# Optimization experiments

Measured on AMD Instinct MI355X. Metric: run time of the kernel, lower is better.

Reference implementation:

```python
import jax, jax.numpy as jnp
import numpy as np
from jax import lax

B, CIN, H, W = 2, 64, 56, 56
CMID, COUT = 128, 128


def _pos_enc(h, w, c, dtype):
    # 2D sinusoidal encoding: first half of channels encode row, second half column.
    def enc1d(L, dim):
        pos = jnp.arange(L, dtype=jnp.float32)[:, None]
        div = jnp.exp(-jnp.log(10000.0) * jnp.arange(0, dim, 2, dtype=jnp.float32) / dim)
        ang = pos * div
        e = jnp.zeros((L, dim), jnp.float32)
        e = e.at[:, 0::2].set(jnp.sin(ang)).at[:, 1::2].set(jnp.cos(ang))
        return e
    ch = c // 2
    eh = enc1d(h, ch)            # (H, ch)
    ew = enc1d(w, c - ch)        # (W, c-ch)
    pe = jnp.concatenate([
        jnp.broadcast_to(eh[:, None, :], (h, w, ch)),
        jnp.broadcast_to(ew[None, :, :], (h, w, c - ch)),
    ], axis=-1)
    return pe.astype(dtype)


def _nbr_idx(L, k, d):
    # NATTEN-style dilated neighborhood indices with border clamping, per dilation
    # residue group. Returns (L, k) int32 indices into [0, L).
    i = jnp.arange(L)
    p, r = i // d, i % d
    Lg = (L - r - 1) // d + 1                      # group length per residue
    start = jnp.clip(p - k // 2, 0, jnp.maximum(Lg - k, 0))
    j = jnp.arange(k)
    idx = r[:, None] + (start[:, None] + j[None, :]) * d
    return jnp.minimum(idx, L - 1)


def setup_inputs() -> dict:
    key = jax.random.key(0)
    ks = jax.random.split(key, 9)
    s3 = 1.0 / np.sqrt(CIN * 9)
    s1 = 1.0 / np.sqrt(CMID)
    return {
        "x": jax.random.normal(ks[0], (B, CIN, H, W), jnp.float32),
        "conv_w": jax.random.normal(ks[1], (CMID, CIN, 3, 3), jnp.float32) * s3,
        "conv_b": jax.random.normal(ks[2], (CMID,), jnp.float32) * 0.01,
        "q_w": jax.random.normal(ks[3], (CMID, CMID), jnp.float32) * s1,
        "q_b": jax.random.normal(ks[4], (CMID,), jnp.float32) * 0.01,
        "k_w": jax.random.normal(ks[5], (CMID, CMID), jnp.float32) * s1,
        "k_b": jax.random.normal(ks[6], (CMID,), jnp.float32) * 0.01,
        "v_w": jax.random.normal(ks[7], (COUT, CMID), jnp.float32) * s1,
        "v_b": jax.random.normal(ks[8], (COUT,), jnp.float32) * 0.01,
        "kernel_size": 7,
        "dilation": 2,
    }


def reference(x, conv_w, conv_b, q_w, q_b, k_w, k_b, v_w, v_b, kernel_size, dilation):
    # shared 3x3 conv projection (SAME padding), NCHW
    sf = lax.conv_general_dilated(x, conv_w, (1, 1), 'SAME',
                                  dimension_numbers=('NCHW', 'OIHW', 'NCHW'))
    sf = sf + conv_b[None, :, None, None]
    sf = jnp.transpose(sf, (0, 2, 3, 1))                      # (B,H,W,Cmid)
    q = jnp.einsum('bhwc,oc->bhwo', sf, q_w) + q_b            # 1x1 convs
    k = jnp.einsum('bhwc,oc->bhwo', sf, k_w) + k_b
    v = jnp.einsum('bhwc,oc->bhwo', sf, v_w) + v_b            # (B,H,W,Cout)
    pe = _pos_enc(q.shape[1], q.shape[2], q.shape[3], q.dtype)
    peb = jnp.broadcast_to(pe[None], q.shape)
    q = jnp.concatenate([q, peb], axis=-1)                    # (B,H,W,2Cmid)
    k = jnp.concatenate([k, peb], axis=-1)

    kk = int(kernel_size)
    dd = int(dilation)
    ih = _nbr_idx(q.shape[1], kk, dd)                         # (H,kk)
    iw = _nbr_idx(q.shape[2], kk, dd)                         # (W,kk)
    # gather dilated neighborhoods: (B,H,W,kk,kk,D)
    knb = k[:, ih[:, None, :, None], iw[None, :, None, :], :]
    vnb = v[:, ih[:, None, :, None], iw[None, :, None, :], :]
    scale = 1.0 / jnp.sqrt(jnp.asarray(q.shape[-1], q.dtype))
    logits = jnp.einsum('bhwd,bhwuvd->bhwuv', q, knb) * scale
    Bq, Hq, Wq = logits.shape[:3]
    attn = jax.nn.softmax(logits.reshape(Bq, Hq, Wq, kk * kk), axis=-1)
    attn = attn.reshape(Bq, Hq, Wq, kk, kk)
    out = jnp.einsum('bhwuv,bhwuvd->bhwd', attn, vnb)         # (B,H,W,Cout)
    return out
```

## Files before the change

kernel.cpp:

```cpp
#include <hip/hip_runtime.h>
#include <hip/hip_bf16.h>
#include <math.h>

#define BB   2
#define HH   56
#define WW   56
#define CIN  64
#define CMID 128

typedef short bf8_t __attribute__((ext_vector_type(8)));
typedef float f4_t  __attribute__((ext_vector_type(4)));
typedef _Float16 h2_t __attribute__((ext_vector_type(2)));
typedef _Float16 h8_t __attribute__((ext_vector_type(8)));

#define QH_OFF  0
#define KH_OFF  401408
#define V_OFF   802816
#define SF_OFF  1605632
#define AS_OFF  2408448
#define WFH_OFF 2408840
#define WFL_OFF 2445704
#define W2H_OFF 2482568
#define W2L_OFF 2507144

__device__ __forceinline__ unsigned short f2bf(float f) {
    unsigned int u = __builtin_bit_cast(unsigned int, f);
    u += 0x7fffu + ((u >> 16) & 1u);
    return (unsigned short)(u >> 16);
}
__device__ __forceinline__ float bf2f(unsigned short h) {
    unsigned int u = ((unsigned int)h) << 16;
    return __builtin_bit_cast(float, u);
}

__global__ __launch_bounds__(256) void prep_w(
    const float* __restrict__ cw, const float* __restrict__ qw,
    const float* __restrict__ kw, const float* __restrict__ vw,
    unsigned short* __restrict__ wfh, unsigned short* __restrict__ wfl,
    unsigned short* __restrict__ w2h, unsigned short* __restrict__ w2l,
    float* __restrict__ As)
{
    int idx = blockIdx.x * 256 + threadIdx.x;
    if (idx < 9 * 2 * 8 * 64 * 8) {
        int j    = idx & 7;
        int lane = (idx >> 3) & 63;
        int o16  = (idx >> 9) & 7;
        int kk32 = (idx >> 12) & 1;
        int seg  = idx >> 13;
        int o = o16 * 16 + (lane & 15);
        int c = kk32 * 32 + (lane >> 4) * 8 + j;
        float wv = cw[(o * 64 + c) * 9 + seg];
        unsigned short hi = f2bf(wv);
        wfh[idx] = hi; wfl[idx] = f2bf(wv - bf2f(hi));
    }
    if (idx < 4 * 24 * 64 * 8) {
        int j    = idx & 7;
        int lane = (idx >> 3) & 63;
        int rest = idx >> 9;
        int n16  = rest % 24;
        int kk32 = rest / 24;
        int n = n16 * 16 + (lane & 15);
        int c = kk32 * 32 + (lane >> 4) * 8 + j;
        int which = n >> 7, o = n & 127;
        const float* src = which == 0 ? qw : (which == 1 ? kw : vw);
        float wv = src[o * 128 + c];
        unsigned short hi = f2bf(wv);
        w2h[idx] = hi; w2l[idx] = f2bf(wv - bf2f(hi));
    }
    if (blockIdx.x == 288) {
        for (int t = threadIdx.x; t < 56 * 7; t += 256) {
            int i = t / 7, j = t % 7;
            int p = i >> 1;
            int start = p - 3;
            if (start < 0) start = 0;
            if (start > 21) start = 21;
            int nidx = (i & 1) + (start + j) * 2;
            float delta = (float)(i - nidx);
            float acc = 0.f;
            for (int u = 0; u < 32; ++u) {
                float d = expf(-9.210340371976184f * (float)u * 0.03125f);
                acc += cosf(delta * d);
            }
            As[t] = acc * 0.0625f;
        }
    }
}

__global__ __launch_bounds__(512) void conv_mfma(
    const float* __restrict__ x,
    const unsigned short* __restrict__ wfh, const unsigned short* __restrict__ wfl,
    const float* __restrict__ cb,
    float* __restrict__ sf)
{
    __shared__ char xsb[2][3 * 66 * 64 * 2];
    const int h   = blockIdx.x;
    const int b   = blockIdx.y;
    const int tid = threadIdx.x;

    for (int idx = tid; idx < 3 * 64 * 66; idx += 512) {
        int dh  = idx / (64 * 66);
        int rem = idx % (64 * 66);
        int c   = rem / 66;
        int row = rem % 66;
        int y   = h + dh - 1;
        int wg  = row - 1;
        float val = 0.f;
        if ((unsigned)y < HH && (unsigned)wg < WW)
            val = x[((b * CIN + c) * HH + y) * WW + wg];
        unsigned short hi = f2bf(val);
        unsigned short lo = f2bf(val - bf2f(hi));
        int byteoff = (((dh * 66 + row) * 64 + c) * 2) ^ ((row & 7) << 4);
        *(unsigned short*)(xsb[0] + byteoff) = hi;
        *(unsigned short*)(xsb[1] + byteoff) = lo;
    }
    __syncthreads();

    const int lane   = tid & 63;
    const int wid    = tid >> 6;
    const int wm     = wid >> 2;
    const int wn     = wid & 3;
    const int lane15 = lane & 15;
    const int lanehi = lane >> 4;

    f4_t acc[2][2] = {};

    for (int seg = 0; seg < 9; ++seg) {
        const int dh = seg / 3, dw = seg % 3;
#pragma unroll
        for (int kk32 = 0; kk32 < 2; ++kk32) {
            bf8_t ah[2], al[2], bh[2], bl[2];
#pragma unroll
            for (int mf = 0; mf < 2; ++mf) {
                int row = wm * 32 + mf * 16 + lane15 + dw;
                int byteoff = (((dh * 66 + row) * 64 + kk32 * 32 + lanehi * 8) * 2)
                              ^ ((row & 7) << 4);
                ah[mf] = *(const bf8_t*)(xsb[0] + byteoff);
                al[mf] = *(const bf8_t*)(xsb[1] + byteoff);
            }
#pragma unroll
            for (int nf = 0; nf < 2; ++nf) {
                int fidx = (((seg * 2 + kk32) * 8 + (wn * 2 + nf)) * 64 + lane) * 8;
                bh[nf] = *(const bf8_t*)(wfh + fidx);
                bl[nf] = *(const bf8_t*)(wfl + fidx);
            }
#pragma unroll
            for (int mf = 0; mf < 2; ++mf)
#pragma unroll
                for (int nf = 0; nf < 2; ++nf) {
                    acc[mf][nf] = __builtin_amdgcn_mfma_f32_16x16x32_bf16(
                        ah[mf], bh[nf], acc[mf][nf], 0, 0, 0);
                    acc[mf][nf] = __builtin_amdgcn_mfma_f32_16x16x32_bf16(
                        al[mf], bh[nf], acc[mf][nf], 0, 0, 0);
                    acc[mf][nf] = __builtin_amdgcn_mfma_f32_16x16x32_bf16(
                        ah[mf], bl[nf], acc[mf][nf], 0, 0, 0);
                }
        }
    }

    const int r4 = lanehi * 4;
#pragma unroll
    for (int mf = 0; mf < 2; ++mf) {
        int wr = wm * 32 + mf * 16 + r4;
#pragma unroll
        for (int nf = 0; nf < 2; ++nf) {
            int o = wn * 32 + nf * 16 + lane15;
            float bias = cb[o];
#pragma unroll
            for (int r = 0; r < 4; ++r) {
                int wpos = wr + r;
                if (wpos < 56)
                    sf[((b * HH + h) * WW + wpos) * CMID + o] = acc[mf][nf][r] + bias;
            }
        }
    }
}

__global__ __launch_bounds__(512) void qkv_mfma(
    const float* __restrict__ sf,
    const unsigned short* __restrict__ w2h, const unsigned short* __restrict__ w2l,
    const float* __restrict__ qb, const float* __restrict__ kb,
    const float* __restrict__ vb,
    _Float16* __restrict__ qh16, _Float16* __restrict__ kh16,
    float* __restrict__ vo)
{
    __shared__ char asb[2][32 * 128 * 2];
    const int p0  = blockIdx.x * 32;
    const int tid = threadIdx.x;

    {
        int row = tid >> 4;
        int c0  = (tid & 15) * 8;
        float4 fa = *(const float4*)(sf + (p0 + row) * 128 + c0);
        float4 fb = *(const float4*)(sf + (p0 + row) * 128 + c0 + 4);
        bf8_t hi, lo;
        float fv[8] = {fa.x, fa.y, fa.z, fa.w, fb.x, fb.y, fb.z, fb.w};
#pragma unroll
        for (int j = 0; j < 8; ++j) {
            unsigned short hj = f2bf(fv[j]);
            hi[j] = (short)hj;
            lo[j] = (short)f2bf(fv[j] - bf2f(hj));
        }
        int byteoff = ((row * 128 + c0) * 2) ^ ((row & 7) << 4);
        *(bf8_t*)(asb[0] + byteoff) = hi;
        *(bf8_t*)(asb[1] + byteoff) = lo;
    }
    __syncthreads();

    const int lane   = tid & 63;
    const int wid    = tid >> 6;
    const int wm     = wid >> 2;
    const int wn     = wid & 3;
    const int lane15 = lane & 15;
    const int lanehi = lane >> 4;

    f4_t acc[6] = {};

#pragma unroll
    for (int kk32 = 0; kk32 < 4; ++kk32) {
        bf8_t ah, al;
        {
            int row = wm * 16 + lane15;
            int byteoff = ((row * 128 + kk32 * 32 + lanehi * 8) * 2) ^ ((row & 7) << 4);
            ah = *(const bf8_t*)(asb[0] + byteoff);
            al = *(const bf8_t*)(asb[1] + byteoff);
        }
#pragma unroll
        for (int nf = 0; nf < 6; ++nf) {
            int fidx = ((kk32 * 24 + wn * 6 + nf) * 64 + lane) * 8;
            bf8_t bhv = *(const bf8_t*)(w2h + fidx);
            bf8_t blv = *(const bf8_t*)(w2l + fidx);
            acc[nf] = __builtin_amdgcn_mfma_f32_16x16x32_bf16(ah, bhv, acc[nf], 0, 0, 0);
            acc[nf] = __builtin_amdgcn_mfma_f32_16x16x32_bf16(al, bhv, acc[nf], 0, 0, 0);
            acc[nf] = __builtin_amdgcn_mfma_f32_16x16x32_bf16(ah, blv, acc[nf], 0, 0, 0);
        }
    }

    const int r4 = lanehi * 4;
#pragma unroll
    for (int nf = 0; nf < 6; ++nf) {
        int n = wn * 96 + nf * 16 + lane15;
        int which = n >> 7;
        int o = n & 127;
        const float* bp = which == 0 ? qb : (which == 1 ? kb : vb);
        float bias = bp[o];
        int pos = p0 + wm * 16 + r4;
#pragma unroll
        for (int r = 0; r < 4; ++r) {
            float val = acc[nf][r] + bias;
            int di = (pos + r) * CMID + o;
            if (which == 0)      qh16[di] = (_Float16)(val * 0.0625f);
            else if (which == 1) kh16[di] = (_Float16)val;
            else                 vo[di]   = val;
        }
    }
}

__global__ __launch_bounds__(256) void attn_tiled(
    const _Float16* __restrict__ qh, const _Float16* __restrict__ kh,
    const float* __restrict__ v, const float* __restrict__ As,
    float* __restrict__ out)
{
    __shared__ char Kb[112 * 256];
    __shared__ char Vb[100 * 256];
    __shared__ char Qb[16 * 256];
    __shared__ float lg[16 * 113];
    __shared__ float awv[4][64];

    const int tid = threadIdx.x;
    int bid = blockIdx.x;
    const int b   = bid / 196; bid %= 196;
    const int par = bid / 49;
    const int t49 = bid % 49;
    const int rh = par >> 1, rw = par & 1;
    const int p0 = (t49 / 7) * 4, q0 = (t49 % 7) * 4;

    int smh = p0 - 3; if (smh < 0) smh = 0; if (smh > 21) smh = 21;
    int smw = q0 - 3; if (smw < 0) smw = 0; if (smw > 21) smw = 21;

    const int rlo = tid >> 4;
    const int t16 = tid & 15;

    {
        int qi = rlo;
        int pp = p0 + (qi >> 2), qq = q0 + (qi & 3);
        int hq = rh + 2 * pp, wq = rw + 2 * qq;
        const char* src = (const char*)(qh + ((b * HH + hq) * WW + wq) * CMID);
        uint4 d = *(const uint4*)(src + t16 * 16);
        *(uint4*)(Qb + qi * 256 + ((t16 * 16) ^ ((qi & 7) << 4))) = d;
    }
    for (int r0 = 0; r0 < 112; r0 += 16) {
        int n = r0 + rlo;
        int i = n / 10, jj = n % 10;
        int ihs = smh + i; if (ihs > 27) ihs = 27;
        int iws = smw + jj; if (iws > 27) iws = 27;
        int ih = rh + 2 * ihs, iw = rw + 2 * iws;
        const char* src = (const char*)(kh + ((b * HH + ih) * WW + iw) * CMID);
        uint4 d = *(const uint4*)(src + t16 * 16);
        *(uint4*)(Kb + n * 256 + ((t16 * 16) ^ ((n & 7) << 4))) = d;
    }
    for (int r0 = 0; r0 < 112; r0 += 16) {
        int n = r0 + rlo;
        if (n < 100) {
            int i = n / 10, jj = n % 10;
            int ihs = smh + i; if (ihs > 27) ihs = 27;
            int iws = smw + jj; if (iws > 27) iws = 27;
            int ih = rh + 2 * ihs, iw = rw + 2 * iws;
            const float* src = v + ((b * HH + ih) * WW + iw) * CMID + t16 * 8;
            float4 f0 = *(const float4*)(src);
            float4 f1 = *(const float4*)(src + 4);
            h8_t d;
            d[0] = (_Float16)f0.x; d[1] = (_Float16)f0.y;
            d[2] = (_Float16)f0.z; d[3] = (_Float16)f0.w;
            d[4] = (_Float16)f1.x; d[5] = (_Float16)f1.y;
            d[6] = (_Float16)f1.z; d[7] = (_Float16)f1.w;
            *(h8_t*)(Vb + n * 256 + t16 * 16) = d;
        }
    }
    __syncthreads();

    const int lane   = tid & 63;
    const int wvid   = tid >> 6;
    const int lane15 = lane & 15;
    const int lanehi = lane >> 4;

    {
        int nfs = wvid * 2;
        int nfe = nfs + 2; if (nfe > 7) nfe = 7;
        for (int nf = nfs; nf < nfe; ++nf) {
            f4_t acc = {};
            int n = nf * 16 + lane15;
#pragma unroll
            for (int kk = 0; kk < 4; ++kk) {
                int koff = kk * 64 + lanehi * 16;
                h8_t a  = *(const h8_t*)(Qb + lane15 * 256 + (koff ^ ((lane15 & 7) << 4)));
                h8_t bb = *(const h8_t*)(Kb + n * 256      + (koff ^ ((n & 7) << 4)));
                acc = __builtin_amdgcn_mfma_f32_16x16x32_f16(a, bb, acc, 0, 0, 0);
            }
#pragma unroll
            for (int r = 0; r < 4; ++r)
                lg[(lanehi * 4 + r) * 113 + n] = acc[r];
        }
    }
    __syncthreads();

    const int u   = lane / 7;
    const int vv2 = lane % 7;

    for (int t = 0; t < 4; ++t) {
        int qi = wvid * 4 + t;
        int pp = p0 + (qi >> 2), qq = q0 + (qi & 3);
        int hq = rh + 2 * pp, wq = rw + 2 * qq;
        int sp = pp - 3; if (sp < 0) sp = 0; if (sp > 21) sp = 21;
        int sq = qq - 3; if (sq < 0) sq = 0; if (sq > 21) sq = 21;
        int ru = sp - smh, rc = sq - smw;

        float logit = -INFINITY;
        if (lane < 49) {
            int n = (ru + u) * 10 + (rc + vv2);
            logit = lg[qi * 113 + n] + As[hq * 7 + u] + As[wq * 7 + vv2];
        }
        float m = logit;
#pragma unroll
        for (int s = 32; s > 0; s >>= 1)
            m = fmaxf(m, __shfl_xor(m, s, 64));
        float e = (lane < 49) ? expf(logit - m) : 0.f;
        float ssum = e;
#pragma unroll
        for (int s = 32; s > 0; s >>= 1)
            ssum += __shfl_xor(ssum, s, 64);
        awv[wvid][lane] = e / ssum;

        float o0 = 0.f, o1 = 0.f;
#pragma unroll
        for (int u2 = 0; u2 < 7; ++u2) {
            int rowb = (ru + u2) * 10 + rc;
#pragma unroll
            for (int v2 = 0; v2 < 7; ++v2) {
                float a2 = awv[wvid][u2 * 7 + v2];
                unsigned pv = *(const unsigned*)(Vb + (rowb + v2) * 256 + lane * 4);
                h2_t ph = __builtin_bit_cast(h2_t, pv);
                o0 += a2 * (float)ph[0];
                o1 += a2 * (float)ph[1];
            }
        }
        int g = (b * HH + hq) * WW + wq;
        *(float2*)(out + g * CMID + lane * 2) = make_float2(o0, o1);
    }
}

extern "C" void kernel_launch(void* const* d_in, const int* in_sizes, int n_in,
                              void* d_out, int out_size, void* d_ws, size_t ws_size,
                              hipStream_t stream)
{
    const float* x  = (const float*)d_in[0];
    const float* cw = (const float*)d_in[1];
    const float* cb = (const float*)d_in[2];
    const float* qw = (const float*)d_in[3];
    const float* qb = (const float*)d_in[4];
    const float* kw = (const float*)d_in[5];
    const float* kb = (const float*)d_in[6];
    const float* vw = (const float*)d_in[7];
    const float* vb = (const float*)d_in[8];

    float* ws = (float*)d_ws;
    _Float16* qhx = (_Float16*)(ws + QH_OFF);
    _Float16* khx = (_Float16*)(ws + KH_OFF);
    float* vx = ws + V_OFF;
    float* sf = ws + SF_OFF;
    float* As = ws + AS_OFF;
    unsigned short* wfh = (unsigned short*)(ws + WFH_OFF);
    unsigned short* wfl = (unsigned short*)(ws + WFL_OFF);
    unsigned short* w2h = (unsigned short*)(ws + W2H_OFF);
    unsigned short* w2l = (unsigned short*)(ws + W2L_OFF);
    float* out = (float*)d_out;

    hipLaunchKernelGGL(prep_w, dim3(289), dim3(256), 0, stream,
                       cw, qw, kw, vw, wfh, wfl, w2h, w2l, As);
    hipLaunchKernelGGL(conv_mfma, dim3(56, 2), dim3(512), 0, stream,
                       x, wfh, wfl, cb, sf);
    hipLaunchKernelGGL(qkv_mfma, dim3(196), dim3(512), 0, stream,
                       sf, w2h, w2l, qb, kb, vb, qhx, khx, vx);
    hipLaunchKernelGGL(attn_tiled, dim3(392), dim3(256), 0, stream,
                       qhx, khx, vx, As, out);
}
```

Measured before the change: 132.6 us.

## Fuse conv and QKV projection into one kernel, store V as fp16

Merges the 3x3 conv and the 1x1 QKV projection into a single kernel. Each block computes a 28-wide half-row of conv output, keeps it in shared memory as split bf16 hi/lo, then runs the QKV MFMAs directly. This removes the fp32 sf round-trip through global memory and one kernel launch. V is now written as fp16, so the attention kernel copies it straight into LDS without converting, which halves V traffic. The grid doubles to 224 blocks but each block does half the conv M-tile, with some halo recompute.

```diff
diff --git a/kernel.cpp b/kernel.cpp
--- a/kernel.cpp
+++ b/kernel.cpp
@@ -15,13 +15,12 @@
 
 #define QH_OFF  0
 #define KH_OFF  401408
-#define V_OFF   802816
-#define SF_OFF  1605632
-#define AS_OFF  2408448
-#define WFH_OFF 2408840
-#define WFL_OFF 2445704
-#define W2H_OFF 2482568
-#define W2L_OFF 2507144
+#define VH_OFF  802816
+#define AS_OFF  1204224
+#define WFH_OFF 1204736
+#define WFL_OFF 1241600
+#define W2H_OFF 1278464
+#define W2L_OFF 1303040
 
 __device__ __forceinline__ unsigned short f2bf(float f) {
     unsigned int u = __builtin_bit_cast(unsigned int, f);
@@ -86,30 +85,37 @@
     }
 }
 
-__global__ __launch_bounds__(512) void conv_mfma(
+__global__ __launch_bounds__(512) void conv_qkv_mfma(
     const float* __restrict__ x,
     const unsigned short* __restrict__ wfh, const unsigned short* __restrict__ wfl,
     const float* __restrict__ cb,
-    float* __restrict__ sf)
+    const unsigned short* __restrict__ w2h, const unsigned short* __restrict__ w2l,
+    const float* __restrict__ qb, const float* __restrict__ kb,
+    const float* __restrict__ vb,
+    _Float16* __restrict__ qh16, _Float16* __restrict__ kh16,
+    _Float16* __restrict__ vh16)
 {
-    __shared__ char xsb[2][3 * 66 * 64 * 2];
-    const int h   = blockIdx.x;
-    const int b   = blockIdx.y;
+    __shared__ char xsb[2][3 * 34 * 64 * 2];
+    __shared__ char sfb[2][32 * 128 * 2];
+    const int wt = blockIdx.x;
+    const int h  = blockIdx.y;
+    const int b  = blockIdx.z;
+    const int w0 = wt * 28;
     const int tid = threadIdx.x;
 
-    for (int idx = tid; idx < 3 * 64 * 66; idx += 512) {
-        int dh  = idx / (64 * 66);
-        int rem = idx % (64 * 66);
-        int c   = rem / 66;
-        int row = rem % 66;
+    for (int idx = tid; idx < 3 * 64 * 34; idx += 512) {
+        int dh  = idx / (64 * 34);
+        int rem = idx % (64 * 34);
+        int c   = rem / 34;
+        int row = rem % 34;
         int y   = h + dh - 1;
-        int wg  = row - 1;
+        int wg  = w0 - 1 + row;
         float val = 0.f;
         if ((unsigned)y < HH && (unsigned)wg < WW)
             val = x[((b * CIN + c) * HH + y) * WW + wg];
         unsigned short hi = f2bf(val);
         unsigned short lo = f2bf(val - bf2f(hi));
-        int byteoff = (((dh * 66 + row) * 64 + c) * 2) ^ ((row & 7) << 4);
+        int byteoff = (((dh * 34 + row) * 64 + c) * 2) ^ ((row & 7) << 4);
         *(unsigned short*)(xsb[0] + byteoff) = hi;
         *(unsigned short*)(xsb[1] + byteoff) = lo;
     }
@@ -122,120 +128,63 @@
     const int lane15 = lane & 15;
     const int lanehi = lane >> 4;
 
-    f4_t acc[2][2] = {};
-
+    f4_t acc[2] = {};
     for (int seg = 0; seg < 9; ++seg) {
         const int dh = seg / 3, dw = seg % 3;
 #pragma unroll
         for (int kk32 = 0; kk32 < 2; ++kk32) {
-            bf8_t ah[2], al[2], bh[2], bl[2];
-#pragma unroll
-            for (int mf = 0; mf < 2; ++mf) {
-                int row = wm * 32 + mf * 16 + lane15 + dw;
-                int byteoff = (((dh * 66 + row) * 64 + kk32 * 32 + lanehi * 8) * 2)
-                              ^ ((row & 7) << 4);
-                ah[mf] = *(const bf8_t*)(xsb[0] + byteoff);
-                al[mf] = *(const bf8_t*)(xsb[1] + byteoff);
-            }
+            int row = wm * 16 + lane15 + dw;
+            int byteoff = (((dh * 34 + row) * 64 + kk32 * 32 + lanehi * 8) * 2)
+                          ^ ((row & 7) << 4);
+            bf8_t ah = *(const bf8_t*)(xsb[0] + byteoff);
+            bf8_t al = *(const bf8_t*)(xsb[1] + byteoff);
 #pragma unroll
             for (int nf = 0; nf < 2; ++nf) {
                 int fidx = (((seg * 2 + kk32) * 8 + (wn * 2 + nf)) * 64 + lane) * 8;
-                bh[nf] = *(const bf8_t*)(wfh + fidx);
-                bl[nf] = *(const bf8_t*)(wfl + fidx);
-            }
-#pragma unroll
-            for (int mf = 0; mf < 2; ++mf)
-#pragma unroll
-                for (int nf = 0; nf < 2; ++nf) {
-                    acc[mf][nf] = __builtin_amdgcn_mfma_f32_16x16x32_bf16(
-                        ah[mf], bh[nf], acc[mf][nf], 0, 0, 0);
-                    acc[mf][nf] = __builtin_amdgcn_mfma_f32_16x16x32_bf16(
-                        al[mf], bh[nf], acc[mf][nf], 0, 0, 0);
-                    acc[mf][nf] = __builtin_amdgcn_mfma_f32_16x16x32_bf16(
-                        ah[mf], bl[nf], acc[mf][nf], 0, 0, 0);
-                }
-        }
-    }
-
-    const int r4 = lanehi * 4;
-#pragma unroll
-    for (int mf = 0; mf < 2; ++mf) {
-        int wr = wm * 32 + mf * 16 + r4;
-#pragma unroll
-        for (int nf = 0; nf < 2; ++nf) {
-            int o = wn * 32 + nf * 16 + lane15;
-            float bias = cb[o];
-#pragma unroll
-            for (int r = 0; r < 4; ++r) {
-                int wpos = wr + r;
-                if (wpos < 56)
-                    sf[((b * HH + h) * WW + wpos) * CMID + o] = acc[mf][nf][r] + bias;
-            }
-        }
-    }
-}
-
-__global__ __launch_bounds__(512) void qkv_mfma(
-    const float* __restrict__ sf,
-    const unsigned short* __restrict__ w2h, const unsigned short* __restrict__ w2l,
-    const float* __restrict__ qb, const float* __restrict__ kb,
-    const float* __restrict__ vb,
-    _Float16* __restrict__ qh16, _Float16* __restrict__ kh16,
-    float* __restrict__ vo)
-{
-    __shared__ char asb[2][32 * 128 * 2];
-    const int p0  = blockIdx.x * 32;
-    const int tid = threadIdx.x;
-
-    {
-        int row = tid >> 4;
-        int c0  = (tid & 15) * 8;
-        float4 fa = *(const float4*)(sf + (p0 + row) * 128 + c0);
-        float4 fb = *(const float4*)(sf + (p0 + row) * 128 + c0 + 4);
-        bf8_t hi, lo;
-        float fv[8] = {fa.x, fa.y, fa.z, fa.w, fb.x, fb.y, fb.z, fb.w};
-#pragma unroll
-        for (int j = 0; j < 8; ++j) {
-            unsigned short hj = f2bf(fv[j]);
-            hi[j] = (short)hj;
-            lo[j] = (short)f2bf(fv[j] - bf2f(hj));
-        }
-        int byteoff = ((row * 128 + c0) * 2) ^ ((row & 7) << 4);
-        *(bf8_t*)(asb[0] + byteoff) = hi;
-        *(bf8_t*)(asb[1] + byteoff) = lo;
+                bf8_t bh = *(const bf8_t*)(wfh + fidx);
+                bf8_t bl = *(const bf8_t*)(wfl + fidx);
+                acc[nf] = __builtin_amdgcn_mfma_f32_16x16x32_bf16(ah, bh, acc[nf], 0, 0, 0);
+                acc[nf] = __builtin_amdgcn_mfma_f32_16x16x32_bf16(al, bh, acc[nf], 0, 0, 0);
+                acc[nf] = __builtin_amdgcn_mfma_f32_16x16x32_bf16(ah, bl, acc[nf], 0, 0, 0);
+            }
+        }
+    }
+
+#pragma unroll
+    for (int nf = 0; nf < 2; ++nf) {
+        int ch = wn * 32 + nf * 16 + lane15;
+        float bias = cb[ch];
+#pragma unroll
+        for (int r = 0; r < 4; ++r) {
+            int m = wm * 16 + lanehi * 4 + r;
+            float val = acc[nf][r] + bias;
+            unsigned short hi = f2bf(val);
+            unsigned short lo = f2bf(val - bf2f(hi));
+            int byteoff = ((m * 128 + ch) * 2) ^ ((m & 7) << 4);
+            *(unsigned short*)(sfb[0] + byteoff) = hi;
+            *(unsigned short*)(sfb[1] + byteoff) = lo;
+        }
     }
     __syncthreads();
 
-    const int lane   = tid & 63;
-    const int wid    = tid >> 6;
-    const int wm     = wid >> 2;
-    const int wn     = wid & 3;
-    const int lane15 = lane & 15;
-    const int lanehi = lane >> 4;
-
-    f4_t acc[6] = {};
-
+    f4_t acc2[6] = {};
 #pragma unroll
     for (int kk32 = 0; kk32 < 4; ++kk32) {
-        bf8_t ah, al;
-        {
-            int row = wm * 16 + lane15;
-            int byteoff = ((row * 128 + kk32 * 32 + lanehi * 8) * 2) ^ ((row & 7) << 4);
-            ah = *(const bf8_t*)(asb[0] + byteoff);
-            al = *(const bf8_t*)(asb[1] + byteoff);
-        }
+        int row = wm * 16 + lane15;
+        int byteoff = ((row * 128 + kk32 * 32 + lanehi * 8) * 2) ^ ((row & 7) << 4);
+        bf8_t ah = *(const bf8_t*)(sfb[0] + byteoff);
+        bf8_t al = *(const bf8_t*)(sfb[1] + byteoff);
 #pragma unroll
         for (int nf = 0; nf < 6; ++nf) {
             int fidx = ((kk32 * 24 + wn * 6 + nf) * 64 + lane) * 8;
-            bf8_t bhv = *(const bf8_t*)(w2h + fidx);
-            bf8_t blv = *(const bf8_t*)(w2l + fidx);
-            acc[nf] = __builtin_amdgcn_mfma_f32_16x16x32_bf16(ah, bhv, acc[nf], 0, 0, 0);
-            acc[nf] = __builtin_amdgcn_mfma_f32_16x16x32_bf16(al, bhv, acc[nf], 0, 0, 0);
-            acc[nf] = __builtin_amdgcn_mfma_f32_16x16x32_bf16(ah, blv, acc[nf], 0, 0, 0);
-        }
-    }
-
-    const int r4 = lanehi * 4;
+            bf8_t bh = *(const bf8_t*)(w2h + fidx);
+            bf8_t bl = *(const bf8_t*)(w2l + fidx);
+            acc2[nf] = __builtin_amdgcn_mfma_f32_16x16x32_bf16(ah, bh, acc2[nf], 0, 0, 0);
+            acc2[nf] = __builtin_amdgcn_mfma_f32_16x16x32_bf16(al, bh, acc2[nf], 0, 0, 0);
+            acc2[nf] = __builtin_amdgcn_mfma_f32_16x16x32_bf16(ah, bl, acc2[nf], 0, 0, 0);
+        }
+    }
+
 #pragma unroll
     for (int nf = 0; nf < 6; ++nf) {
         int n = wn * 96 + nf * 16 + lane15;
@@ -243,21 +192,24 @@
         int o = n & 127;
         const float* bp = which == 0 ? qb : (which == 1 ? kb : vb);
         float bias = bp[o];
-        int pos = p0 + wm * 16 + r4;
 #pragma unroll
         for (int r = 0; r < 4; ++r) {
-            float val = acc[nf][r] + bias;
-            int di = (pos + r) * CMID + o;
-            if (which == 0)      qh16[di] = (_Float16)(val * 0.0625f);
-            else if (which == 1) kh16[di] = (_Float16)val;
-            else                 vo[di]   = val;
+            int m = wm * 16 + lanehi * 4 + r;
+            int wpos = w0 + m;
+            if (wpos < WW) {
+                float val = acc2[nf][r] + bias;
+                int di = ((b * HH + h) * WW + wpos) * CMID + o;
+                if (which == 0)      qh16[di] = (_Float16)(val * 0.0625f);
+                else if (which == 1) kh16[di] = (_Float16)val;
+                else                 vh16[di] = (_Float16)val;
+            }
         }
     }
 }
 
 __global__ __launch_bounds__(256) void attn_tiled(
     const _Float16* __restrict__ qh, const _Float16* __restrict__ kh,
-    const float* __restrict__ v, const float* __restrict__ As,
+    const _Float16* __restrict__ vh, const float* __restrict__ As,
     float* __restrict__ out)
 {
     __shared__ char Kb[112 * 256];
@@ -305,15 +257,9 @@
             int ihs = smh + i; if (ihs > 27) ihs = 27;
             int iws = smw + jj; if (iws > 27) iws = 27;
             int ih = rh + 2 * ihs, iw = rw + 2 * iws;
-            const float* src = v + ((b * HH + ih) * WW + iw) * CMID + t16 * 8;
-            float4 f0 = *(const float4*)(src);
-            float4 f1 = *(const float4*)(src + 4);
-            h8_t d;
-            d[0] = (_Float16)f0.x; d[1] = (_Float16)f0.y;
-            d[2] = (_Float16)f0.z; d[3] = (_Float16)f0.w;
-            d[4] = (_Float16)f1.x; d[5] = (_Float16)f1.y;
-            d[6] = (_Float16)f1.z; d[7] = (_Float16)f1.w;
-            *(h8_t*)(Vb + n * 256 + t16 * 16) = d;
+            const char* src = (const char*)(vh + ((b * HH + ih) * WW + iw) * CMID);
+            uint4 d = *(const uint4*)(src + t16 * 16);
+            *(uint4*)(Vb + n * 256 + t16 * 16) = d;
         }
     }
     __syncthreads();
@@ -405,8 +351,7 @@
     float* ws = (float*)d_ws;
     _Float16* qhx = (_Float16*)(ws + QH_OFF);
     _Float16* khx = (_Float16*)(ws + KH_OFF);
-    float* vx = ws + V_OFF;
-    float* sf = ws + SF_OFF;
+    _Float16* vhx = (_Float16*)(ws + VH_OFF);
     float* As = ws + AS_OFF;
     unsigned short* wfh = (unsigned short*)(ws + WFH_OFF);
     unsigned short* wfl = (unsigned short*)(ws + WFL_OFF);
@@ -416,10 +361,8 @@
 
     hipLaunchKernelGGL(prep_w, dim3(289), dim3(256), 0, stream,
                        cw, qw, kw, vw, wfh, wfl, w2h, w2l, As);
-    hipLaunchKernelGGL(conv_mfma, dim3(56, 2), dim3(512), 0, stream,
-                       x, wfh, wfl, cb, sf);
-    hipLaunchKernelGGL(qkv_mfma, dim3(196), dim3(512), 0, stream,
-                       sf, w2h, w2l, qb, kb, vb, qhx, khx, vx);
+    hipLaunchKernelGGL(conv_qkv_mfma, dim3(2, 56, 2), dim3(512), 0, stream,
+                       x, wfh, wfl, cb, w2h, w2l, qb, kb, vb, qhx, khx, vhx);
     hipLaunchKernelGGL(attn_tiled, dim3(392), dim3(256), 0, stream,
-                       qhx, khx, vx, As, out);
-}
+                       qhx, khx, vhx, As, out);
+}
```

New measurement: 117.1 us. -11.7%, faster.
